# Performance work log

Hardware: AMD Instinct MI355X
Metric: run time of the kernel (lower is better)

The kernel has to match this reference:

```python
import jax, jax.numpy as jnp
import numpy as np

EPS = 0.01

def _hos_pool(x):
    # x: [B, C, T] -> [B, 4C]; matches torch mean/std(unbiased)/skew/kurt over time
    T = x.shape[-1]
    mean = jnp.mean(x, axis=-1)                              # [B, C]
    centered = x - mean[..., None]                           # [B, C, T]
    var_b = jnp.sum(centered * centered, axis=-1) / (T - 1)  # unbiased variance
    std = jnp.sqrt(var_b)
    norm = centered / jnp.maximum(std, EPS)[..., None]
    n2 = norm * norm
    skew = jnp.mean(n2 * norm, axis=-1)
    kurt = jnp.mean(n2 * n2, axis=-1)
    return jnp.concatenate([mean, std, skew, kurt], axis=-1)  # [B, 4C]


def setup_inputs() -> dict:
    key = jax.random.key(0)
    ks = jax.random.split(key, 6)
    B, C, T, BR = 32, 512, 4000, 2
    sc = 1.0 / np.sqrt(4 * C)
    return {
        "x_a": jax.random.normal(ks[0], (B, C, T), dtype=jnp.float32),
        "x_b": jax.random.normal(ks[1], (B, C, T), dtype=jnp.float32),
        "W1": jax.random.normal(ks[2], (C, 4 * C), dtype=jnp.float32) * sc,
        "b1": jax.random.normal(ks[3], (C,), dtype=jnp.float32) * sc,
        "W2": jax.random.normal(ks[4], (BR, C, C), dtype=jnp.float32) * (1.0 / np.sqrt(C)),
        "b2": jax.random.normal(ks[5], (BR, C), dtype=jnp.float32) * (1.0 / np.sqrt(C)),
    }


def reference(x_a, x_b, W1, b1, W2, b2):
    # f: [B, 2, C, T]
    f = jnp.stack([x_a, x_b], axis=1)
    x_sum = x_a + x_b                                        # [B, C, T]
    stats = _hos_pool(x_sum)                                 # [B, 4C]
    h = stats @ W1.T + b1                                    # [B, C_hidden]
    # per-branch gate logits: [B, BR, C]
    s = jnp.einsum("bh,koh->bko", h, W2) + b2[None, :, :]
    s = jax.nn.softmax(s, axis=1)[..., None]                 # [B, BR, C, 1]
    return jnp.sum(f * s, axis=1)                            # [B, C, T]
```

## Files before the change

kernel.cpp:

```cpp
#include <hip/hip_runtime.h>
#include <math.h>

#define T_LEN 4000
#define T4    1000
#define BDIM  256
#define EPS   0.01f

typedef float v4f __attribute__((ext_vector_type(4)));

__device__ __forceinline__ float waveReduceSum(float v) {
    #pragma unroll
    for (int off = 32; off > 0; off >>= 1) v += __shfl_down(v, off, 64);
    return v;
}

__global__ __launch_bounds__(BDIM) void stats_kernel(
    const float* __restrict__ xa, const float* __restrict__ xb,
    float* __restrict__ stats, int C) {
    __shared__ float red[4][4];

    const int r = blockIdx.x;
    const int b = r / C;
    const int c = r - b * C;
    const int tid = threadIdx.x;
    const int wave = tid >> 6, lane = tid & 63;

    const v4f* a4 = (const v4f*)(xa + (size_t)r * T_LEN);
    const v4f* b4 = (const v4f*)(xb + (size_t)r * T_LEN);

    const bool has4 = (tid < (T4 - 3 * BDIM));
    v4f av0 = a4[tid];
    v4f bv0 = b4[tid];
    v4f av1 = a4[tid + BDIM];
    v4f bv1 = b4[tid + BDIM];
    v4f av2 = a4[tid + 2 * BDIM];
    v4f bv2 = b4[tid + 2 * BDIM];
    v4f av3 = {0.f, 0.f, 0.f, 0.f};
    v4f bv3 = {0.f, 0.f, 0.f, 0.f};
    if (has4) { av3 = a4[tid + 3 * BDIM]; bv3 = b4[tid + 3 * BDIM]; }

    float s1 = 0.f, s2 = 0.f, s3 = 0.f, s4 = 0.f;
    #define ACC(av, bv)                                                      \
    {                                                                        \
        float x0 = av.x + bv.x, x1 = av.y + bv.y,                            \
              x2 = av.z + bv.z, x3 = av.w + bv.w;                            \
        float q0 = x0 * x0, q1 = x1 * x1, q2 = x2 * x2, q3 = x3 * x3;        \
        s1 += (x0 + x1) + (x2 + x3);                                         \
        s2 += (q0 + q1) + (q2 + q3);                                         \
        s3 += (q0 * x0 + q1 * x1) + (q2 * x2 + q3 * x3);                     \
        s4 += (q0 * q0 + q1 * q1) + (q2 * q2 + q3 * q3);                     \
    }
    ACC(av0, bv0)
    ACC(av1, bv1)
    ACC(av2, bv2)
    ACC(av3, bv3)
    #undef ACC

    s1 = waveReduceSum(s1);
    s2 = waveReduceSum(s2);
    s3 = waveReduceSum(s3);
    s4 = waveReduceSum(s4);
    if (lane == 0) { red[wave][0] = s1; red[wave][1] = s2; red[wave][2] = s3; red[wave][3] = s4; }
    __syncthreads();

    if (tid == 0) {
        float S1 = red[0][0] + red[1][0] + red[2][0] + red[3][0];
        float S2 = red[0][1] + red[1][1] + red[2][1] + red[3][1];
        float S3 = red[0][2] + red[1][2] + red[2][2] + red[3][2];
        float S4 = red[0][3] + red[1][3] + red[2][3] + red[3][3];
        const float invT = 1.0f / T_LEN;
        float mean = S1 * invT;
        float m = mean, m2c = m * m;
        float M2 = S2 - S1 * m;
        float M3 = S3 - 3.0f * m * S2 + 2.0f * m2c * S1;
        float M4 = S4 - 4.0f * m * S3 + 6.0f * m2c * S2 - 3.0f * m2c * m * S1;
        float var_b = M2 / (float)(T_LEN - 1);
        float sd = sqrtf(fmaxf(var_b, 0.0f));
        float d = fmaxf(sd, EPS);
        float inv = 1.0f / d;
        float inv2 = inv * inv;
        float skew = (M3 * invT) * inv2 * inv;
        float kurt = (M4 * invT) * inv2 * inv2;
        float* srow = stats + (size_t)b * (4 * C);
        srow[c]         = mean;
        srow[C + c]     = sd;
        srow[2 * C + c] = skew;
        srow[3 * C + c] = kurt;
    }
}

__global__ __launch_bounds__(BDIM) void h_kernel(
    const float* __restrict__ stats, const float* __restrict__ W1,
    const float* __restrict__ b1, float* __restrict__ h, int C) {
    __shared__ __align__(16) float sst[2048];
    const int H = 4 * C;
    const int groups = C / 4;
    const int b = blockIdx.x / groups;
    const int grp = blockIdx.x - b * groups;
    const int tid = threadIdx.x;
    const int wave = tid >> 6, lane = tid & 63;
    const int o = grp * 4 + wave;

    const v4f* src4 = (const v4f*)(stats + (size_t)b * H);
    v4f* sst4 = (v4f*)sst;
    for (int i = tid; i < H / 4; i += BDIM) sst4[i] = src4[i];
    __syncthreads();

    const v4f* s4 = (const v4f*)sst;
    const v4f* w4 = (const v4f*)(W1 + (size_t)o * H);
    float acc = 0.f;
    #pragma unroll
    for (int it = 0; it < 8; ++it) {
        int idx = it * 64 + lane;
        v4f w = w4[idx];
        v4f s = s4[idx];
        acc += (w.x * s.x + w.y * s.y) + (w.z * s.z + w.w * s.w);
    }
    acc = waveReduceSum(acc);
    if (lane == 0) h[(size_t)b * C + o] = acc + b1[o];
}

__global__ __launch_bounds__(BDIM) void gate_kernel(
    const float* __restrict__ h, const float* __restrict__ W2,
    const float* __restrict__ b2, float* __restrict__ g, int C) {
    __shared__ __align__(16) float hs[512];
    const int groups = C / 4;
    const int b  = blockIdx.x / groups;
    const int cg = blockIdx.x - b * groups;
    const int tid = threadIdx.x;
    const int wave = tid >> 6, lane = tid & 63;
    const int c = cg * 4 + wave;

    for (int i = tid; i < C; i += BDIM) hs[i] = h[(size_t)b * C + i];
    __syncthreads();

    const v4f* h4 = (const v4f*)hs;
    const v4f* w0 = (const v4f*)(W2 + (size_t)c * C);
    const v4f* w1 = (const v4f*)(W2 + (size_t)C * C + (size_t)c * C);
    float l0 = 0.f, l1 = 0.f;
    #pragma unroll
    for (int it = 0; it < 2; ++it) {
        int i = it * 64 + lane;
        v4f hv = h4[i];
        v4f a0 = w0[i];
        v4f a1 = w1[i];
        l0 += (hv.x * a0.x + hv.y * a0.y) + (hv.z * a0.z + hv.w * a0.w);
        l1 += (hv.x * a1.x + hv.y * a1.y) + (hv.z * a1.z + hv.w * a1.w);
    }
    l0 = waveReduceSum(l0);
    l1 = waveReduceSum(l1);
    if (lane == 0) {
        float L0 = l0 + b2[c];
        float L1 = l1 + b2[C + c];
        g[(size_t)b * C + c] = 1.0f / (1.0f + expf(L1 - L0));
    }
}

__global__ __launch_bounds__(BDIM) void blend_kernel(
    const float* __restrict__ xa, const float* __restrict__ xb,
    const float* __restrict__ g, float* __restrict__ out) {
    const int r = (int)gridDim.x - 1 - (int)blockIdx.x;
    const int tid = threadIdx.x;

    const v4f* a4 = (const v4f*)(xa + (size_t)r * T_LEN);
    const v4f* b4 = (const v4f*)(xb + (size_t)r * T_LEN);
    v4f* o4 = (v4f*)(out + (size_t)r * T_LEN);

    const bool has4 = (tid < (T4 - 3 * BDIM));
    v4f A0 = __builtin_nontemporal_load(a4 + tid);
    v4f B0 = __builtin_nontemporal_load(b4 + tid);
    v4f A1 = __builtin_nontemporal_load(a4 + tid + BDIM);
    v4f B1 = __builtin_nontemporal_load(b4 + tid + BDIM);
    v4f A2 = __builtin_nontemporal_load(a4 + tid + 2 * BDIM);
    v4f B2 = __builtin_nontemporal_load(b4 + tid + 2 * BDIM);
    v4f A3 = {0.f, 0.f, 0.f, 0.f};
    v4f B3 = {0.f, 0.f, 0.f, 0.f};
    if (has4) {
        A3 = __builtin_nontemporal_load(a4 + tid + 3 * BDIM);
        B3 = __builtin_nontemporal_load(b4 + tid + 3 * BDIM);
    }

    const float gv = g[r];
    const float hg = 1.0f - gv;

    v4f O0 = A0 * gv + B0 * hg;
    v4f O1 = A1 * gv + B1 * hg;
    v4f O2 = A2 * gv + B2 * hg;
    __builtin_nontemporal_store(O0, o4 + tid);
    __builtin_nontemporal_store(O1, o4 + tid + BDIM);
    __builtin_nontemporal_store(O2, o4 + tid + 2 * BDIM);
    if (has4) {
        v4f O3 = A3 * gv + B3 * hg;
        __builtin_nontemporal_store(O3, o4 + tid + 3 * BDIM);
    }
}

extern "C" void kernel_launch(void* const* d_in, const int* in_sizes, int n_in,
                              void* d_out, int out_size, void* d_ws, size_t ws_size,
                              hipStream_t stream) {
    const float* xa = (const float*)d_in[0];
    const float* xb = (const float*)d_in[1];
    const float* W1 = (const float*)d_in[2];
    const float* b1 = (const float*)d_in[3];
    const float* W2 = (const float*)d_in[4];
    const float* b2 = (const float*)d_in[5];
    float* out = (float*)d_out;

    const int C = in_sizes[3];
    const int B = in_sizes[0] / (C * T_LEN);

    float* stats = (float*)d_ws;
    float* h     = stats + (size_t)B * 4 * C;
    float* g     = stats;

    stats_kernel<<<B * C, BDIM, 0, stream>>>(xa, xb, stats, C);
    h_kernel<<<B * (C / 4), BDIM, 0, stream>>>(stats, W1, b1, h, C);
    gate_kernel<<<B * (C / 4), BDIM, 0, stream>>>(h, W2, b2, g, C);
    blend_kernel<<<B * C, BDIM, 0, stream>>>(xa, xb, g, out);
}
```

Measured before the change: 681.4 us.

## Pipeline batch groups: fuse next group's stats with current group's blend

Splits the batch into groups of 8 and launches a fused kernel whose blocks blend group g while computing the stats of group g+1, with the small h and gate kernels run per group. Revisiting each group's inputs soon after they were read for stats is meant to let the blend reads hit in the last-level cache, and overlapping the two streaming phases is meant to hide the serialized tail. The price is more kernel launches and small serialized MLP kernels per group, and the fused kernel's mix of block types may be uneven. The gate buffer moves to its own workspace region so it no longer overwrites stats that later groups still need.

```diff
diff --git a/kernel.cpp b/kernel.cpp
--- a/kernel.cpp
+++ b/kernel.cpp
@@ -14,12 +14,10 @@
     return v;
 }
 
-__global__ __launch_bounds__(BDIM) void stats_kernel(
-    const float* __restrict__ xa, const float* __restrict__ xb,
-    float* __restrict__ stats, int C) {
+__device__ __forceinline__ void stats_row(
+    const float* __restrict__ xa, const float* __restrict__ xb,
+    float* __restrict__ stats, int C, int r) {
     __shared__ float red[4][4];
-
-    const int r = blockIdx.x;
     const int b = r / C;
     const int c = r - b * C;
     const int tid = threadIdx.x;
@@ -89,14 +87,75 @@
     }
 }
 
+__device__ __forceinline__ void blend_row(
+    const float* __restrict__ xa, const float* __restrict__ xb,
+    const float* __restrict__ g, float* __restrict__ out, int r) {
+    const int tid = threadIdx.x;
+    const v4f* a4 = (const v4f*)(xa + (size_t)r * T_LEN);
+    const v4f* b4 = (const v4f*)(xb + (size_t)r * T_LEN);
+    v4f* o4 = (v4f*)(out + (size_t)r * T_LEN);
+
+    const bool has4 = (tid < (T4 - 3 * BDIM));
+    v4f A0 = __builtin_nontemporal_load(a4 + tid);
+    v4f B0 = __builtin_nontemporal_load(b4 + tid);
+    v4f A1 = __builtin_nontemporal_load(a4 + tid + BDIM);
+    v4f B1 = __builtin_nontemporal_load(b4 + tid + BDIM);
+    v4f A2 = __builtin_nontemporal_load(a4 + tid + 2 * BDIM);
+    v4f B2 = __builtin_nontemporal_load(b4 + tid + 2 * BDIM);
+    v4f A3 = {0.f, 0.f, 0.f, 0.f};
+    v4f B3 = {0.f, 0.f, 0.f, 0.f};
+    if (has4) {
+        A3 = __builtin_nontemporal_load(a4 + tid + 3 * BDIM);
+        B3 = __builtin_nontemporal_load(b4 + tid + 3 * BDIM);
+    }
+
+    const float gv = g[r];
+    const float hg = 1.0f - gv;
+
+    v4f O0 = A0 * gv + B0 * hg;
+    v4f O1 = A1 * gv + B1 * hg;
+    v4f O2 = A2 * gv + B2 * hg;
+    __builtin_nontemporal_store(O0, o4 + tid);
+    __builtin_nontemporal_store(O1, o4 + tid + BDIM);
+    __builtin_nontemporal_store(O2, o4 + tid + 2 * BDIM);
+    if (has4) {
+        v4f O3 = A3 * gv + B3 * hg;
+        __builtin_nontemporal_store(O3, o4 + tid + 3 * BDIM);
+    }
+}
+
+__global__ __launch_bounds__(BDIM) void stats_kernel(
+    const float* __restrict__ xa, const float* __restrict__ xb,
+    float* __restrict__ stats, int C, int rowBase) {
+    stats_row(xa, xb, stats, C, rowBase + (int)blockIdx.x);
+}
+
+__global__ __launch_bounds__(BDIM) void blend_kernel(
+    const float* __restrict__ xa, const float* __restrict__ xb,
+    const float* __restrict__ g, float* __restrict__ out, int rowBase) {
+    blend_row(xa, xb, g, out, rowBase + (int)gridDim.x - 1 - (int)blockIdx.x);
+}
+
+__global__ __launch_bounds__(BDIM) void fused_kernel(
+    const float* __restrict__ xa, const float* __restrict__ xb,
+    float* __restrict__ stats, const float* __restrict__ g,
+    float* __restrict__ out, int C, int statsRowBase, int blendRowBase,
+    int nBlend) {
+    if ((int)blockIdx.x < nBlend) {
+        blend_row(xa, xb, g, out, blendRowBase + nBlend - 1 - (int)blockIdx.x);
+    } else {
+        stats_row(xa, xb, stats, C, statsRowBase + (int)blockIdx.x - nBlend);
+    }
+}
+
 __global__ __launch_bounds__(BDIM) void h_kernel(
     const float* __restrict__ stats, const float* __restrict__ W1,
-    const float* __restrict__ b1, float* __restrict__ h, int C) {
+    const float* __restrict__ b1, float* __restrict__ h, int C, int bBase) {
     __shared__ __align__(16) float sst[2048];
     const int H = 4 * C;
     const int groups = C / 4;
-    const int b = blockIdx.x / groups;
-    const int grp = blockIdx.x - b * groups;
+    const int b = bBase + (int)blockIdx.x / groups;
+    const int grp = (int)blockIdx.x % groups;
     const int tid = threadIdx.x;
     const int wave = tid >> 6, lane = tid & 63;
     const int o = grp * 4 + wave;
@@ -122,11 +181,11 @@
 
 __global__ __launch_bounds__(BDIM) void gate_kernel(
     const float* __restrict__ h, const float* __restrict__ W2,
-    const float* __restrict__ b2, float* __restrict__ g, int C) {
+    const float* __restrict__ b2, float* __restrict__ g, int C, int bBase) {
     __shared__ __align__(16) float hs[512];
     const int groups = C / 4;
-    const int b  = blockIdx.x / groups;
-    const int cg = blockIdx.x - b * groups;
+    const int b  = bBase + (int)blockIdx.x / groups;
+    const int cg = (int)blockIdx.x % groups;
     const int tid = threadIdx.x;
     const int wave = tid >> 6, lane = tid & 63;
     const int c = cg * 4 + wave;
@@ -156,45 +215,6 @@
     }
 }
 
-__global__ __launch_bounds__(BDIM) void blend_kernel(
-    const float* __restrict__ xa, const float* __restrict__ xb,
-    const float* __restrict__ g, float* __restrict__ out) {
-    const int r = (int)gridDim.x - 1 - (int)blockIdx.x;
-    const int tid = threadIdx.x;
-
-    const v4f* a4 = (const v4f*)(xa + (size_t)r * T_LEN);
-    const v4f* b4 = (const v4f*)(xb + (size_t)r * T_LEN);
-    v4f* o4 = (v4f*)(out + (size_t)r * T_LEN);
-
-    const bool has4 = (tid < (T4 - 3 * BDIM));
-    v4f A0 = __builtin_nontemporal_load(a4 + tid);
-    v4f B0 = __builtin_nontemporal_load(b4 + tid);
-    v4f A1 = __builtin_nontemporal_load(a4 + tid + BDIM);
-    v4f B1 = __builtin_nontemporal_load(b4 + tid + BDIM);
-    v4f A2 = __builtin_nontemporal_load(a4 + tid + 2 * BDIM);
-    v4f B2 = __builtin_nontemporal_load(b4 + tid + 2 * BDIM);
-    v4f A3 = {0.f, 0.f, 0.f, 0.f};
-    v4f B3 = {0.f, 0.f, 0.f, 0.f};
-    if (has4) {
-        A3 = __builtin_nontemporal_load(a4 + tid + 3 * BDIM);
-        B3 = __builtin_nontemporal_load(b4 + tid + 3 * BDIM);
-    }
-
-    const float gv = g[r];
-    const float hg = 1.0f - gv;
-
-    v4f O0 = A0 * gv + B0 * hg;
-    v4f O1 = A1 * gv + B1 * hg;
-    v4f O2 = A2 * gv + B2 * hg;
-    __builtin_nontemporal_store(O0, o4 + tid);
-    __builtin_nontemporal_store(O1, o4 + tid + BDIM);
-    __builtin_nontemporal_store(O2, o4 + tid + 2 * BDIM);
-    if (has4) {
-        v4f O3 = A3 * gv + B3 * hg;
-        __builtin_nontemporal_store(O3, o4 + tid + 3 * BDIM);
-    }
-}
-
 extern "C" void kernel_launch(void* const* d_in, const int* in_sizes, int n_in,
                               void* d_out, int out_size, void* d_ws, size_t ws_size,
                               hipStream_t stream) {
@@ -209,12 +229,27 @@
     const int C = in_sizes[3];
     const int B = in_sizes[0] / (C * T_LEN);
 
+    int G = 8;
+    if (B % G) G = B;
+    const int nGroups = B / G;
+    const int rowsPG  = G * C;
+
     float* stats = (float*)d_ws;
     float* h     = stats + (size_t)B * 4 * C;
-    float* g     = stats;
-
-    stats_kernel<<<B * C, BDIM, 0, stream>>>(xa, xb, stats, C);
-    h_kernel<<<B * (C / 4), BDIM, 0, stream>>>(stats, W1, b1, h, C);
-    gate_kernel<<<B * (C / 4), BDIM, 0, stream>>>(h, W2, b2, g, C);
-    blend_kernel<<<B * C, BDIM, 0, stream>>>(xa, xb, g, out);
-}
+    float* gbuf  = h + (size_t)B * C;
+
+    stats_kernel<<<rowsPG, BDIM, 0, stream>>>(xa, xb, stats, C, 0);
+    for (int g = 0; g < nGroups; ++g) {
+        h_kernel<<<G * (C / 4), BDIM, 0, stream>>>(stats, W1, b1, h, C, g * G);
+        gate_kernel<<<G * (C / 4), BDIM, 0, stream>>>(h, W2, b2, gbuf, C, g * G);
+        if (g + 1 < nGroups) {
+            fused_kernel<<<2 * rowsPG, BDIM, 0, stream>>>(
+                xa, xb, stats, gbuf, out, C,
+                (g + 1) * rowsPG , g * rowsPG ,
+                rowsPG);
+        } else {
+            blend_kernel<<<rowsPG, BDIM, 0, stream>>>(xa, xb, gbuf, out,
+                                                      g * rowsPG);
+        }
+    }
+}
```

Result: no change. 683.2 us (+0.3%).
